# Optimization experiments

Hardware: AMD Instinct MI355X
Metric: run time of the kernel (lower is better)

## Reference

```python
import jax, jax.numpy as jnp
import numpy as np

D = 128
EPS = 1e-5

def group_norm1(x, gamma, beta):
    # GroupNorm with num_groups=1 over channel dim of [N, C]
    mu = jnp.mean(x, axis=-1, keepdims=True)
    var = jnp.mean(jnp.square(x - mu), axis=-1, keepdims=True)
    xhat = (x - mu) * jax.lax.rsqrt(var + EPS)
    return xhat * gamma + beta

def setup_inputs() -> dict:
    key = jax.random.key(0)
    ks = jax.random.split(key, 12)
    N_ctx, N_tgt, E = 40000, 40000, 640000
    s = 0.09  # ~1/sqrt(128) weight scale
    inp = {
        'context_feat': jax.random.normal(ks[0], (N_ctx, D), jnp.float32),
        'target_feat': jax.random.normal(ks[1], (N_tgt, D), jnp.float32),
        'context_pose': jax.random.normal(ks[2], (N_ctx, 4), jnp.float32),
        'target_pose': jax.random.normal(ks[3], (N_tgt, 4), jnp.float32),
        'W_input': s * jax.random.normal(ks[4], (D, D), jnp.float32),
        'W_rp': 0.5 * jax.random.normal(ks[5], (4, D), jnp.float32),
        'b_rp': jnp.zeros((D,), jnp.float32),
        'W_c1': s * jax.random.normal(ks[6], (2 * D, D), jnp.float32),
        'g_c1': jnp.ones((D,), jnp.float32),
        'b_c1': jnp.zeros((D,), jnp.float32),
        'W_c2': s * jax.random.normal(ks[7], (D, D), jnp.float32),
        'g_n': jnp.ones((D,), jnp.float32),
        'b_n': jnp.zeros((D,), jnp.float32),
        'W_m1': s * jax.random.normal(ks[8], (D, D), jnp.float32),
        'g_m1': jnp.ones((D,), jnp.float32),
        'bm1': jnp.zeros((D,), jnp.float32),
        'W_m2': s * jax.random.normal(ks[9], (D, D), jnp.float32),
        'g_m2': jnp.ones((D,), jnp.float32),
        'bm2': jnp.zeros((D,), jnp.float32),
        'hi': jax.random.randint(ks[10], (E,), 0, N_ctx, jnp.int32),
        'wi': jax.random.randint(ks[11], (E,), 0, N_tgt, jnp.int32),
    }
    return inp

def reference(context_feat, target_feat, context_pose, target_pose,
              W_input, W_rp, b_rp, W_c1, g_c1, b_c1, W_c2,
              g_n, b_n, W_m1, g_m1, bm1, W_m2, g_m2, bm2, hi, wi):
    # relpose: Linear(4,128) + ReLU on relative pose of each (context, target) edge
    dist_feat = context_pose[hi] - target_pose[wi]                 # [E, 4]
    dist_feat = jax.nn.relu(dist_feat @ W_rp + b_rp)               # [E, 128]
    # ctx: Linear(256,128,GN,ReLU) -> Linear(128,128, no bias)
    ctx = jnp.concatenate([context_feat[hi], dist_feat], axis=-1)  # [E, 256]
    ctx = jax.nn.relu(group_norm1(ctx @ W_c1, g_c1, b_c1))
    ctx = ctx @ W_c2                                               # [E, 128]
    # input linear + index_add scatter into targets
    tf = target_feat @ W_input                                     # [N_tgt, 128]
    tf = tf + jax.ops.segment_sum(ctx, wi, num_segments=target_feat.shape[0])
    tf = jax.nn.relu(group_norm1(tf, g_n, b_n))
    # mlp: Linear(GN,ReLU) -> Linear(GN, no act)
    tf = jax.nn.relu(group_norm1(tf @ W_m1, g_m1, bm1))
    tf = group_norm1(tf @ W_m2, g_m2, bm2)
    # residual + relu
    return jax.nn.relu(tf + target_feat)
```

## Files before the change

### kernel.cpp

```cpp
#include <hip/hip_runtime.h>

#define D 128
#define EPSV 1e-5f

typedef __attribute__((ext_vector_type(8))) __bf16 bf16x8;
typedef __attribute__((ext_vector_type(4))) float f32x4;

__device__ __forceinline__ ushort f2bf(float x) {
  unsigned u = __float_as_uint(x);
  u += 0x7fffu + ((u >> 16) & 1u);
  return (ushort)(u >> 16);
}
__device__ __forceinline__ unsigned cvtpk(float lo, float hi) {
  unsigned r;
  asm("v_cvt_pk_bf16_f32 %0, %1, %2" : "=v"(r) : "v"(lo), "v"(hi));
  return r;
}
__device__ __forceinline__ int yidx(int row, int col) {
  return row * 128 + (col ^ ((row & 7) << 3));
}

__global__ void k_cvt(const float* __restrict__ Wc1, const float* __restrict__ Wc2,
                      ushort* __restrict__ WF1, ushort* __restrict__ WF2) {
  int o = blockIdx.x * 256 + threadIdx.x;
  if (o < 32768) {
    int j = o & 7, col = (o >> 3) & 127, gg = (o >> 10) & 3, kc = o >> 12;
    WF1[o] = f2bf(Wc1[(kc * 32 + gg * 8 + j) * 128 + col]);
  } else {
    int o2 = o - 32768;
    if (o2 < 16384) {
      int j = o2 & 7, col = (o2 >> 3) & 127, gg = (o2 >> 10) & 3, kc = o2 >> 12;
      WF2[o2] = f2bf(Wc2[(kc * 32 + gg * 8 + j) * 128 + col]);
    }
  }
}

__global__ void k_cvtf(const float* __restrict__ cf, ushort* __restrict__ cb,
                       int n8) {
  int i = blockIdx.x * 256 + threadIdx.x;
  if (i < n8) {
    float4 f0 = *(const float4*)(cf + (size_t)i * 8);
    float4 f1 = *(const float4*)(cf + (size_t)i * 8 + 4);
    uint4 p;
    p.x = cvtpk(f0.x, f0.y); p.y = cvtpk(f0.z, f0.w);
    p.z = cvtpk(f1.x, f1.y); p.w = cvtpk(f1.z, f1.w);
    *(uint4*)(cb + (size_t)i * 8) = p;
  }
}

template <bool BF16CF>
__global__ __launch_bounds__(256, 4) void k_edge(
    const float* __restrict__ cfeat, const ushort* __restrict__ cfb,
    const float* __restrict__ cpose, const float* __restrict__ tpose,
    const float* __restrict__ Wrp, const float* __restrict__ brp,
    const float* __restrict__ gc1, const float* __restrict__ bc1,
    const ushort* __restrict__ WF1, const ushort* __restrict__ WF2,
    const int* __restrict__ hi, const int* __restrict__ wi,
    float* __restrict__ acc, int E) {
  __shared__ ushort Ybuf[128 * 128];
  __shared__ float gnbuf[2][128][2];
  __shared__ int wl[128];

  const int t = threadIdx.x;
  const int lane = t & 63;
  const int wv = t >> 6;
  const int wm = wv >> 1, wn = wv & 1;
  const int s = lane & 15, g = lane >> 4;
  const int e0 = blockIdx.x * 128;

  if (t < 128) wl[t] = wi[min(e0 + t, E - 1)];

  int hl[4];
#pragma unroll
  for (int m = 0; m < 4; ++m)
    hl[m] = hi[min(e0 + wm * 64 + m * 16 + s, E - 1)];

  {
    const int e = t >> 1;
    const int jh = (t & 1) * 64;
    const int ge = min(e0 + e, E - 1);
    const int h = hi[ge], w = wi[ge];
    float4 cp = *(const float4*)(cpose + (size_t)h * 4);
    float4 tp = *(const float4*)(tpose + (size_t)w * 4);
    const float d0 = cp.x - tp.x, d1 = cp.y - tp.y;
    const float d2 = cp.z - tp.z, d3 = cp.w - tp.w;
#pragma unroll
    for (int q = 0; q < 16; ++q) {
      const int j = jh + q * 4;
      float4 b  = *(const float4*)(brp + j);
      float4 w0 = *(const float4*)(Wrp + j);
      float4 w1 = *(const float4*)(Wrp + D + j);
      float4 w2 = *(const float4*)(Wrp + 2 * D + j);
      float4 w3 = *(const float4*)(Wrp + 3 * D + j);
      float r0 = fmaxf(b.x + d0 * w0.x + d1 * w1.x + d2 * w2.x + d3 * w3.x, 0.f);
      float r1 = fmaxf(b.y + d0 * w0.y + d1 * w1.y + d2 * w2.y + d3 * w3.y, 0.f);
      float r2 = fmaxf(b.z + d0 * w0.z + d1 * w1.z + d2 * w2.z + d3 * w3.z, 0.f);
      float r3 = fmaxf(b.w + d0 * w0.w + d1 * w1.w + d2 * w2.w + d3 * w3.w, 0.f);
      *(uint2*)&Ybuf[yidx(e, j)] = make_uint2(cvtpk(r0, r1), cvtpk(r2, r3));
    }
  }

  auto bfrag = [&](const ushort* WF, int kc, int n) {
    return *(const bf16x8*)&WF[(((kc * 4 + g) * 128) + wn * 64 + n * 16 + s) * 8];
  };

  f32x4 acc1[4][4];
#pragma unroll
  for (int m = 0; m < 4; ++m)
#pragma unroll
    for (int n = 0; n < 4; ++n) acc1[m][n] = (f32x4){0.f, 0.f, 0.f, 0.f};

  for (int kc = 0; kc < 4; ++kc) {
    bf16x8 a[4];
    if (BF16CF) {
#pragma unroll
      for (int m = 0; m < 4; ++m)
        a[m] = *(const bf16x8*)(cfb + (size_t)hl[m] * D + kc * 32 + g * 8);
    } else {
#pragma unroll
      for (int m = 0; m < 4; ++m) {
        const float* src = cfeat + (size_t)hl[m] * D + kc * 32 + g * 8;
        float4 f0 = *(const float4*)src;
        float4 f1 = *(const float4*)(src + 4);
        union { uint4 u; bf16x8 v; } cv;
        cv.u.x = cvtpk(f0.x, f0.y); cv.u.y = cvtpk(f0.z, f0.w);
        cv.u.z = cvtpk(f1.x, f1.y); cv.u.w = cvtpk(f1.z, f1.w);
        a[m] = cv.v;
      }
    }
#pragma unroll
    for (int n = 0; n < 4; ++n) {
      bf16x8 b = bfrag(WF1, kc, n);
#pragma unroll
      for (int m = 0; m < 4; ++m)
        acc1[m][n] =
            __builtin_amdgcn_mfma_f32_16x16x32_bf16(a[m], b, acc1[m][n], 0, 0, 0);
    }
  }

  __syncthreads();

  for (int kc = 4; kc < 8; ++kc) {
    bf16x8 a[4];
#pragma unroll
    for (int m = 0; m < 4; ++m)
      a[m] = *(const bf16x8*)
          &Ybuf[yidx(wm * 64 + m * 16 + s, (kc - 4) * 32 + g * 8)];
#pragma unroll
    for (int n = 0; n < 4; ++n) {
      bf16x8 b = bfrag(WF1, kc, n);
#pragma unroll
      for (int m = 0; m < 4; ++m)
        acc1[m][n] =
            __builtin_amdgcn_mfma_f32_16x16x32_bf16(a[m], b, acc1[m][n], 0, 0, 0);
    }
  }

#pragma unroll
  for (int m = 0; m < 4; ++m) {
#pragma unroll
    for (int reg = 0; reg < 4; ++reg) {
      float p1 = acc1[m][0][reg] + acc1[m][1][reg] + acc1[m][2][reg] +
                 acc1[m][3][reg];
      float p2 = acc1[m][0][reg] * acc1[m][0][reg] +
                 acc1[m][1][reg] * acc1[m][1][reg] +
                 acc1[m][2][reg] * acc1[m][2][reg] +
                 acc1[m][3][reg] * acc1[m][3][reg];
#pragma unroll
      for (int msk = 1; msk < 16; msk <<= 1) {
        p1 += __shfl_xor(p1, msk, 64);
        p2 += __shfl_xor(p2, msk, 64);
      }
      if (s == 0) {
        const int row = wm * 64 + m * 16 + g * 4 + reg;
        *(float2*)&gnbuf[wn][row][0] = make_float2(p1, p2);
      }
    }
  }
  __syncthreads();

  {
    float gcl[4], bcl[4];
#pragma unroll
    for (int n = 0; n < 4; ++n) {
      gcl[n] = gc1[wn * 64 + n * 16 + s];
      bcl[n] = bc1[wn * 64 + n * 16 + s];
    }
#pragma unroll
    for (int m = 0; m < 4; ++m) {
#pragma unroll
      for (int reg = 0; reg < 4; ++reg) {
        const int row = wm * 64 + m * 16 + g * 4 + reg;
        float2 q0 = *(const float2*)&gnbuf[0][row][0];
        float2 q1 = *(const float2*)&gnbuf[1][row][0];
        const float mean = (q0.x + q1.x) * (1.f / 128.f);
        const float var = (q0.y + q1.y) * (1.f / 128.f) - mean * mean;
        const float rstd = rsqrtf(var + EPSV);
#pragma unroll
        for (int n = 0; n < 4; ++n) {
          float y = fmaxf((acc1[m][n][reg] - mean) * rstd * gcl[n] + bcl[n], 0.f);
          Ybuf[yidx(row, wn * 64 + n * 16 + s)] = (ushort)cvtpk(y, y);
        }
      }
    }
  }
  __syncthreads();

  f32x4 acc2[4][4];
#pragma unroll
  for (int m = 0; m < 4; ++m)
#pragma unroll
    for (int n = 0; n < 4; ++n) acc2[m][n] = (f32x4){0.f, 0.f, 0.f, 0.f};

  for (int kc = 0; kc < 4; ++kc) {
    bf16x8 a[4];
#pragma unroll
    for (int m = 0; m < 4; ++m)
      a[m] = *(const bf16x8*)&Ybuf[yidx(wm * 64 + m * 16 + s, kc * 32 + g * 8)];
#pragma unroll
    for (int n = 0; n < 4; ++n) {
      bf16x8 b = bfrag(WF2, kc, n);
#pragma unroll
      for (int m = 0; m < 4; ++m)
        acc2[m][n] =
            __builtin_amdgcn_mfma_f32_16x16x32_bf16(a[m], b, acc2[m][n], 0, 0, 0);
    }
  }

#pragma unroll
  for (int m = 0; m < 4; ++m) {
#pragma unroll
    for (int reg = 0; reg < 4; ++reg) {
      const int rl = wm * 64 + m * 16 + g * 4 + reg;
      if (e0 + rl < E) {
        const int w = wl[rl];
        float* base = acc + (size_t)w * D + wn * 64 + s;
#pragma unroll
        for (int n = 0; n < 4; ++n)
          unsafeAtomicAdd(base + n * 16, acc2[m][n][reg]);
      }
    }
  }
}

__device__ __forceinline__ void reduce16(float& a, float& b) {
#pragma unroll
  for (int w = 1; w < 16; w <<= 1) {
    a += __shfl_xor(a, w, 64);
    b += __shfl_xor(b, w, 64);
  }
}

__global__ __launch_bounds__(256, 2) void k_input(
    const float* __restrict__ tfeat, const float* __restrict__ Wi,
    float* __restrict__ acc, int N) {
  __shared__ float Wbuf[64][132];
  __shared__ float xt[64][132];
  const int t = threadIdx.x;
  const int r = t >> 4, s = t & 15, j0 = s * 8;
  const int row0 = blockIdx.x * 64;

  for (int idx = t; idx < 64 * 32; idx += 256) {
    int rr = idx >> 5, c4 = idx & 31;
    int grow = row0 + rr;
    float4 v = make_float4(0.f, 0.f, 0.f, 0.f);
    if (grow < N) v = *(const float4*)(tfeat + (size_t)grow * D + c4 * 4);
    *(float4*)&xt[rr][c4 * 4] = v;
  }

  float a[4][8] = {};
  for (int kc = 0; kc < 2; ++kc) {
    __syncthreads();
    for (int idx = t; idx < 64 * 32; idx += 256) {
      int kk = idx >> 5, c4 = idx & 31;
      *(float4*)&Wbuf[kk][c4 * 4] =
          *(const float4*)(Wi + (size_t)(kc * 64 + kk) * D + c4 * 4);
    }
    __syncthreads();
#pragma unroll 4
    for (int kk = 0; kk < 64; ++kk) {
      float4 w0 = *(const float4*)&Wbuf[kk][j0];
      float4 w1 = *(const float4*)&Wbuf[kk][j0 + 4];
#pragma unroll
      for (int i = 0; i < 4; ++i) {
        float xv = xt[r + 16 * i][kc * 64 + kk];
        a[i][0] += xv * w0.x; a[i][1] += xv * w0.y;
        a[i][2] += xv * w0.z; a[i][3] += xv * w0.w;
        a[i][4] += xv * w1.x; a[i][5] += xv * w1.y;
        a[i][6] += xv * w1.z; a[i][7] += xv * w1.w;
      }
    }
  }
#pragma unroll
  for (int i = 0; i < 4; ++i) {
    int row = row0 + r + 16 * i;
    if (row < N) {
      *(float4*)(acc + (size_t)row * D + j0) =
          make_float4(a[i][0], a[i][1], a[i][2], a[i][3]);
      *(float4*)(acc + (size_t)row * D + j0 + 4) =
          make_float4(a[i][4], a[i][5], a[i][6], a[i][7]);
    }
  }
}

__global__ __launch_bounds__(256, 2) void k_node(
    const float* __restrict__ tfeat,
    const float* __restrict__ gn, const float* __restrict__ bn,
    const float* __restrict__ Wm1, const float* __restrict__ gm1,
    const float* __restrict__ bm1,
    const float* __restrict__ Wm2, const float* __restrict__ gm2,
    const float* __restrict__ bm2,
    float* __restrict__ acc, int N) {
  __shared__ float Wbuf[64][132];
  __shared__ float xt[64][132];
  const int t = threadIdx.x;
  const int r = t >> 4, s = t & 15, j0 = s * 8;
  const int row0 = blockIdx.x * 64;

  auto stageW = [&](const float* W, int kc) {
    for (int idx = t; idx < 64 * 32; idx += 256) {
      int kk = idx >> 5, c4 = idx & 31;
      *(float4*)&Wbuf[kk][c4 * 4] =
          *(const float4*)(W + (size_t)(kc * 64 + kk) * D + c4 * 4);
    }
  };
  auto gemm = [&](float (&a)[4][8], int kc) {
#pragma unroll 4
    for (int kk = 0; kk < 64; ++kk) {
      float4 w0 = *(const float4*)&Wbuf[kk][j0];
      float4 w1 = *(const float4*)&Wbuf[kk][j0 + 4];
#pragma unroll
      for (int i = 0; i < 4; ++i) {
        float xv = xt[r + 16 * i][kc * 64 + kk];
        a[i][0] += xv * w0.x; a[i][1] += xv * w0.y;
        a[i][2] += xv * w0.z; a[i][3] += xv * w0.w;
        a[i][4] += xv * w1.x; a[i][5] += xv * w1.y;
        a[i][6] += xv * w1.z; a[i][7] += xv * w1.w;
      }
    }
  };

  {
    float gv[8], bv[8];
#pragma unroll
    for (int m = 0; m < 8; ++m) { gv[m] = gn[j0 + m]; bv[m] = bn[j0 + m]; }
#pragma unroll
    for (int i = 0; i < 4; ++i) {
      int row = row0 + r + 16 * i;
      float v[8] = {};
      if (row < N) {
        float4 v0 = *(const float4*)(acc + (size_t)row * D + j0);
        float4 v1 = *(const float4*)(acc + (size_t)row * D + j0 + 4);
        v[0] = v0.x; v[1] = v0.y; v[2] = v0.z; v[3] = v0.w;
        v[4] = v1.x; v[5] = v1.y; v[6] = v1.z; v[7] = v1.w;
      }
      float s1 = 0.f, s2 = 0.f;
#pragma unroll
      for (int m = 0; m < 8; ++m) { s1 += v[m]; s2 += v[m] * v[m]; }
      reduce16(s1, s2);
      float mean = s1 * (1.f / 128.f);
      float var = s2 * (1.f / 128.f) - mean * mean;
      float rstd = rsqrtf(var + EPSV);
#pragma unroll
      for (int m = 0; m < 8; ++m)
        xt[r + 16 * i][j0 + m] = fmaxf((v[m] - mean) * rstd * gv[m] + bv[m], 0.f);
    }
  }

  float a[4][8] = {};
  for (int kc = 0; kc < 2; ++kc) {
    __syncthreads();
    stageW(Wm1, kc);
    __syncthreads();
    gemm(a, kc);
  }
  __syncthreads();
  {
    float gv[8], bv[8];
#pragma unroll
    for (int m = 0; m < 8; ++m) { gv[m] = gm1[j0 + m]; bv[m] = bm1[j0 + m]; }
#pragma unroll
    for (int i = 0; i < 4; ++i) {
      float s1 = 0.f, s2 = 0.f;
#pragma unroll
      for (int m = 0; m < 8; ++m) { s1 += a[i][m]; s2 += a[i][m] * a[i][m]; }
      reduce16(s1, s2);
      float mean = s1 * (1.f / 128.f);
      float var = s2 * (1.f / 128.f) - mean * mean;
      float rstd = rsqrtf(var + EPSV);
#pragma unroll
      for (int m = 0; m < 8; ++m)
        xt[r + 16 * i][j0 + m] =
            fmaxf((a[i][m] - mean) * rstd * gv[m] + bv[m], 0.f);
    }
  }

  float a2[4][8] = {};
  for (int kc = 0; kc < 2; ++kc) {
    __syncthreads();
    stageW(Wm2, kc);
    __syncthreads();
    gemm(a2, kc);
  }
  {
    float gv[8], bv[8];
#pragma unroll
    for (int m = 0; m < 8; ++m) { gv[m] = gm2[j0 + m]; bv[m] = bm2[j0 + m]; }
#pragma unroll
    for (int i = 0; i < 4; ++i) {
      int row = row0 + r + 16 * i;
      float s1 = 0.f, s2 = 0.f;
#pragma unroll
      for (int m = 0; m < 8; ++m) { s1 += a2[i][m]; s2 += a2[i][m] * a2[i][m]; }
      reduce16(s1, s2);
      float mean = s1 * (1.f / 128.f);
      float var = s2 * (1.f / 128.f) - mean * mean;
      float rstd = rsqrtf(var + EPSV);
      if (row < N) {
        float o[8];
#pragma unroll
        for (int m = 0; m < 8; ++m) {
          float x = (a2[i][m] - mean) * rstd * gv[m] + bv[m];
          o[m] = fmaxf(x + tfeat[(size_t)row * D + j0 + m], 0.f);
        }
        *(float4*)(acc + (size_t)row * D + j0) =
            make_float4(o[0], o[1], o[2], o[3]);
        *(float4*)(acc + (size_t)row * D + j0 + 4) =
            make_float4(o[4], o[5], o[6], o[7]);
      }
    }
  }
}

extern "C" void kernel_launch(void* const* d_in, const int* in_sizes, int n_in,
                              void* d_out, int out_size, void* d_ws,
                              size_t ws_size, hipStream_t stream) {
  const float* cfeat = (const float*)d_in[0];
  const float* tfeat = (const float*)d_in[1];
  const float* cpose = (const float*)d_in[2];
  const float* tpose = (const float*)d_in[3];
  const float* Wi    = (const float*)d_in[4];
  const float* Wrp   = (const float*)d_in[5];
  const float* brp   = (const float*)d_in[6];
  const float* Wc1   = (const float*)d_in[7];
  const float* gc1   = (const float*)d_in[8];
  const float* bc1   = (const float*)d_in[9];
  const float* Wc2   = (const float*)d_in[10];
  const float* gn    = (const float*)d_in[11];
  const float* bn    = (const float*)d_in[12];
  const float* Wm1   = (const float*)d_in[13];
  const float* gm1   = (const float*)d_in[14];
  const float* bm1   = (const float*)d_in[15];
  const float* Wm2   = (const float*)d_in[16];
  const float* gm2   = (const float*)d_in[17];
  const float* bm2   = (const float*)d_in[18];
  const int* hi      = (const int*)d_in[19];
  const int* wi      = (const int*)d_in[20];

  const int N = in_sizes[1] / D;
  const int E = in_sizes[19];
  const int CFE = in_sizes[0];
  float* out = (float*)d_out;

  uint8_t* ws = (uint8_t*)d_ws;
  ushort* WF1 = (ushort*)ws;
  ushort* WF2 = (ushort*)(ws + 65536);
  ushort* cfb = (ushort*)(ws + 98304);
  const bool bf16cf = ws_size >= 98304 + (size_t)CFE * 2;

  const int nbN = (N + 63) / 64;
  const int nbE = (E + 127) / 128;

  k_cvt<<<192, 256, 0, stream>>>(Wc1, Wc2, WF1, WF2);
  if (bf16cf) k_cvtf<<<(CFE / 8 + 255) / 256, 256, 0, stream>>>(cfeat, cfb, CFE / 8);
  k_input<<<nbN, 256, 0, stream>>>(tfeat, Wi, out, N);
  if (bf16cf)
    k_edge<true><<<nbE, 256, 0, stream>>>(cfeat, cfb, cpose, tpose, Wrp, brp,
                                          gc1, bc1, WF1, WF2, hi, wi, out, E);
  else
    k_edge<false><<<nbE, 256, 0, stream>>>(cfeat, cfb, cpose, tpose, Wrp, brp,
                                           gc1, bc1, WF1, WF2, hi, wi, out, E);
  k_node<<<nbN, 256, 0, stream>>>(tfeat, gn, bn, Wm1, gm1, bm1, Wm2, gm2, bm2,
                                  out, N);
}
```

Baseline: 476.3 us.

## Scatter pre-W_c2 activations in bf16 and apply W_c2 per node

Uses linearity of segment_sum: the edge kernel now scatters the post-GroupNorm ReLU activations with packed bf16 atomics into a zeroed node buffer S, instead of running the second 128x128 GEMM per edge and scattering fp32 atomics. The node kernel loads S, multiplies it by W_c2, and adds the input projection before the first GroupNorm. This removes one edge-level GEMM (E=640k rows versus N=40k) and halves the atomic traffic and count. The cost is bf16 accumulation precision in the atomics and an extra memset plus a node-level GEMM.

```diff
diff --git a/kernel.cpp b/kernel.cpp
--- a/kernel.cpp
+++ b/kernel.cpp
@@ -16,22 +16,18 @@
   asm("v_cvt_pk_bf16_f32 %0, %1, %2" : "=v"(r) : "v"(lo), "v"(hi));
   return r;
 }
+__device__ __forceinline__ float bf2f(ushort u) {
+  return __uint_as_float((unsigned)u << 16);
+}
 __device__ __forceinline__ int yidx(int row, int col) {
   return row * 128 + (col ^ ((row & 7) << 3));
 }
 
-__global__ void k_cvt(const float* __restrict__ Wc1, const float* __restrict__ Wc2,
-                      ushort* __restrict__ WF1, ushort* __restrict__ WF2) {
+__global__ void k_cvt(const float* __restrict__ Wc1, ushort* __restrict__ WF1) {
   int o = blockIdx.x * 256 + threadIdx.x;
   if (o < 32768) {
     int j = o & 7, col = (o >> 3) & 127, gg = (o >> 10) & 3, kc = o >> 12;
     WF1[o] = f2bf(Wc1[(kc * 32 + gg * 8 + j) * 128 + col]);
-  } else {
-    int o2 = o - 32768;
-    if (o2 < 16384) {
-      int j = o2 & 7, col = (o2 >> 3) & 127, gg = (o2 >> 10) & 3, kc = o2 >> 12;
-      WF2[o2] = f2bf(Wc2[(kc * 32 + gg * 8 + j) * 128 + col]);
-    }
   }
 }
 
@@ -54,9 +50,9 @@
     const float* __restrict__ cpose, const float* __restrict__ tpose,
     const float* __restrict__ Wrp, const float* __restrict__ brp,
     const float* __restrict__ gc1, const float* __restrict__ bc1,
-    const ushort* __restrict__ WF1, const ushort* __restrict__ WF2,
+    const ushort* __restrict__ WF1,
     const int* __restrict__ hi, const int* __restrict__ wi,
-    float* __restrict__ acc, int E) {
+    ushort* __restrict__ S, int E) {
   __shared__ ushort Ybuf[128 * 128];
   __shared__ float gnbuf[2][128][2];
   __shared__ int wl[128];
@@ -100,8 +96,8 @@
     }
   }
 
-  auto bfrag = [&](const ushort* WF, int kc, int n) {
-    return *(const bf16x8*)&WF[(((kc * 4 + g) * 128) + wn * 64 + n * 16 + s) * 8];
+  auto bfrag = [&](int kc, int n) {
+    return *(const bf16x8*)&WF1[(((kc * 4 + g) * 128) + wn * 64 + n * 16 + s) * 8];
   };
 
   f32x4 acc1[4][4];
@@ -130,7 +126,7 @@
     }
 #pragma unroll
     for (int n = 0; n < 4; ++n) {
-      bf16x8 b = bfrag(WF1, kc, n);
+      bf16x8 b = bfrag(kc, n);
 #pragma unroll
       for (int m = 0; m < 4; ++m)
         acc1[m][n] =
@@ -148,7 +144,7 @@
           &Ybuf[yidx(wm * 64 + m * 16 + s, (kc - 4) * 32 + g * 8)];
 #pragma unroll
     for (int n = 0; n < 4; ++n) {
-      bf16x8 b = bfrag(WF1, kc, n);
+      bf16x8 b = bfrag(kc, n);
 #pragma unroll
       for (int m = 0; m < 4; ++m)
         acc1[m][n] =
@@ -186,6 +182,7 @@
       gcl[n] = gc1[wn * 64 + n * 16 + s];
       bcl[n] = bc1[wn * 64 + n * 16 + s];
     }
+    const int odd = s & 1;
 #pragma unroll
     for (int m = 0; m < 4; ++m) {
 #pragma unroll
@@ -196,48 +193,27 @@
         const float mean = (q0.x + q1.x) * (1.f / 128.f);
         const float var = (q0.y + q1.y) * (1.f / 128.f) - mean * mean;
         const float rstd = rsqrtf(var + EPSV);
+        float yv[4], pv[4];
 #pragma unroll
         for (int n = 0; n < 4; ++n) {
-          float y = fmaxf((acc1[m][n][reg] - mean) * rstd * gcl[n] + bcl[n], 0.f);
-          Ybuf[yidx(row, wn * 64 + n * 16 + s)] = (ushort)cvtpk(y, y);
+          yv[n] = fmaxf((acc1[m][n][reg] - mean) * rstd * gcl[n] + bcl[n], 0.f);
+          pv[n] = __shfl_xor(yv[n], 1, 64);
         }
-      }
-    }
-  }
-  __syncthreads();
-
-  f32x4 acc2[4][4];
-#pragma unroll
-  for (int m = 0; m < 4; ++m)
-#pragma unroll
-    for (int n = 0; n < 4; ++n) acc2[m][n] = (f32x4){0.f, 0.f, 0.f, 0.f};
-
-  for (int kc = 0; kc < 4; ++kc) {
-    bf16x8 a[4];
-#pragma unroll
-    for (int m = 0; m < 4; ++m)
-      a[m] = *(const bf16x8*)&Ybuf[yidx(wm * 64 + m * 16 + s, kc * 32 + g * 8)];
-#pragma unroll
-    for (int n = 0; n < 4; ++n) {
-      bf16x8 b = bfrag(WF2, kc, n);
-#pragma unroll
-      for (int m = 0; m < 4; ++m)
-        acc2[m][n] =
-            __builtin_amdgcn_mfma_f32_16x16x32_bf16(a[m], b, acc2[m][n], 0, 0, 0);
-    }
-  }
-
-#pragma unroll
-  for (int m = 0; m < 4; ++m) {
-#pragma unroll
-    for (int reg = 0; reg < 4; ++reg) {
-      const int rl = wm * 64 + m * 16 + g * 4 + reg;
-      if (e0 + rl < E) {
-        const int w = wl[rl];
-        float* base = acc + (size_t)w * D + wn * 64 + s;
-#pragma unroll
-        for (int n = 0; n < 4; ++n)
-          unsafeAtomicAdd(base + n * 16, acc2[m][n][reg]);
+        if (e0 + row < E) {
+          const int w = wl[row];
+          float vA = odd ? yv[2] : yv[0], pA = odd ? pv[2] : pv[0];
+          float vB = odd ? yv[3] : yv[1], pB = odd ? pv[3] : pv[1];
+          unsigned dA = odd ? cvtpk(pA, vA) : cvtpk(vA, pA);
+          unsigned dB = odd ? cvtpk(pB, vB) : cvtpk(vB, pB);
+          const int colA = wn * 64 + (odd ? 32 : 0) + (s & ~1);
+          unsigned long long aA =
+              (unsigned long long)(S + (size_t)w * D + colA);
+          unsigned long long aB = aA + 32;
+          asm volatile("global_atomic_pk_add_bf16 %0, %1, off"
+                       :: "v"(aA), "v"(dA) : "memory");
+          asm volatile("global_atomic_pk_add_bf16 %0, %1, off"
+                       :: "v"(aB), "v"(dB) : "memory");
+        }
       }
     }
   }
@@ -304,7 +280,8 @@
 }
 
 __global__ __launch_bounds__(256, 2) void k_node(
-    const float* __restrict__ tfeat,
+    const float* __restrict__ tfeat, const ushort* __restrict__ S,
+    const float* __restrict__ Wc2,
     const float* __restrict__ gn, const float* __restrict__ bn,
     const float* __restrict__ Wm1, const float* __restrict__ gm1,
     const float* __restrict__ bm1,
@@ -339,46 +316,10 @@
       }
     }
   };
-
-  {
+  auto gnorm = [&](float (&a)[4][8], const float* gv_, const float* bv_) {
     float gv[8], bv[8];
 #pragma unroll
-    for (int m = 0; m < 8; ++m) { gv[m] = gn[j0 + m]; bv[m] = bn[j0 + m]; }
-#pragma unroll
-    for (int i = 0; i < 4; ++i) {
-      int row = row0 + r + 16 * i;
-      float v[8] = {};
-      if (row < N) {
-        float4 v0 = *(const float4*)(acc + (size_t)row * D + j0);
-        float4 v1 = *(const float4*)(acc + (size_t)row * D + j0 + 4);
-        v[0] = v0.x; v[1] = v0.y; v[2] = v0.z; v[3] = v0.w;
-        v[4] = v1.x; v[5] = v1.y; v[6] = v1.z; v[7] = v1.w;
-      }
-      float s1 = 0.f, s2 = 0.f;
-#pragma unroll
-      for (int m = 0; m < 8; ++m) { s1 += v[m]; s2 += v[m] * v[m]; }
-      reduce16(s1, s2);
-      float mean = s1 * (1.f / 128.f);
-      float var = s2 * (1.f / 128.f) - mean * mean;
-      float rstd = rsqrtf(var + EPSV);
-#pragma unroll
-      for (int m = 0; m < 8; ++m)
-        xt[r + 16 * i][j0 + m] = fmaxf((v[m] - mean) * rstd * gv[m] + bv[m], 0.f);
-    }
-  }
-
-  float a[4][8] = {};
-  for (int kc = 0; kc < 2; ++kc) {
-    __syncthreads();
-    stageW(Wm1, kc);
-    __syncthreads();
-    gemm(a, kc);
-  }
-  __syncthreads();
-  {
-    float gv[8], bv[8];
-#pragma unroll
-    for (int m = 0; m < 8; ++m) { gv[m] = gm1[j0 + m]; bv[m] = bm1[j0 + m]; }
+    for (int m = 0; m < 8; ++m) { gv[m] = gv_[j0 + m]; bv[m] = bv_[j0 + m]; }
 #pragma unroll
     for (int i = 0; i < 4; ++i) {
       float s1 = 0.f, s2 = 0.f;
@@ -393,7 +334,57 @@
         xt[r + 16 * i][j0 + m] =
             fmaxf((a[i][m] - mean) * rstd * gv[m] + bv[m], 0.f);
     }
-  }
+  };
+
+  for (int idx = t; idx < 64 * 16; idx += 256) {
+    int rr = idx >> 4, c8 = (idx & 15) * 8;
+    int grow = row0 + rr;
+    if (grow < N) {
+      uint4 p = *(const uint4*)(S + (size_t)grow * D + c8);
+      xt[rr][c8 + 0] = bf2f((ushort)(p.x & 0xffff));
+      xt[rr][c8 + 1] = bf2f((ushort)(p.x >> 16));
+      xt[rr][c8 + 2] = bf2f((ushort)(p.y & 0xffff));
+      xt[rr][c8 + 3] = bf2f((ushort)(p.y >> 16));
+      xt[rr][c8 + 4] = bf2f((ushort)(p.z & 0xffff));
+      xt[rr][c8 + 5] = bf2f((ushort)(p.z >> 16));
+      xt[rr][c8 + 6] = bf2f((ushort)(p.w & 0xffff));
+      xt[rr][c8 + 7] = bf2f((ushort)(p.w >> 16));
+    } else {
+#pragma unroll
+      for (int m = 0; m < 8; ++m) xt[rr][c8 + m] = 0.f;
+    }
+  }
+
+  float a0[4][8] = {};
+#pragma unroll
+  for (int i = 0; i < 4; ++i) {
+    int row = row0 + r + 16 * i;
+    if (row < N) {
+      float4 v0 = *(const float4*)(acc + (size_t)row * D + j0);
+      float4 v1 = *(const float4*)(acc + (size_t)row * D + j0 + 4);
+      a0[i][0] = v0.x; a0[i][1] = v0.y; a0[i][2] = v0.z; a0[i][3] = v0.w;
+      a0[i][4] = v1.x; a0[i][5] = v1.y; a0[i][6] = v1.z; a0[i][7] = v1.w;
+    }
+  }
+
+  for (int kc = 0; kc < 2; ++kc) {
+    __syncthreads();
+    stageW(Wc2, kc);
+    __syncthreads();
+    gemm(a0, kc);
+  }
+  __syncthreads();
+  gnorm(a0, gn, bn);
+
+  float a[4][8] = {};
+  for (int kc = 0; kc < 2; ++kc) {
+    __syncthreads();
+    stageW(Wm1, kc);
+    __syncthreads();
+    gemm(a, kc);
+  }
+  __syncthreads();
+  gnorm(a, gm1, bm1);
 
   float a2[4][8] = {};
   for (int kc = 0; kc < 2; ++kc) {
@@ -464,22 +455,25 @@
 
   uint8_t* ws = (uint8_t*)d_ws;
   ushort* WF1 = (ushort*)ws;
-  ushort* WF2 = (ushort*)(ws + 65536);
-  ushort* cfb = (ushort*)(ws + 98304);
-  const bool bf16cf = ws_size >= 98304 + (size_t)CFE * 2;
+  ushort* S   = (ushort*)(ws + 65536);
+  const size_t sBytes = (size_t)N * D * 2;
+  ushort* cfb = (ushort*)(ws + 65536 + sBytes);
+  const bool bf16cf = ws_size >= 65536 + sBytes + (size_t)CFE * 2;
 
   const int nbN = (N + 63) / 64;
   const int nbE = (E + 127) / 128;
 
-  k_cvt<<<192, 256, 0, stream>>>(Wc1, Wc2, WF1, WF2);
-  if (bf16cf) k_cvtf<<<(CFE / 8 + 255) / 256, 256, 0, stream>>>(cfeat, cfb, CFE / 8);
+  hipMemsetAsync(S, 0, sBytes, stream);
+  k_cvt<<<128, 256, 0, stream>>>(Wc1, WF1);
+  if (bf16cf)
+    k_cvtf<<<(CFE / 8 + 255) / 256, 256, 0, stream>>>(cfeat, cfb, CFE / 8);
   k_input<<<nbN, 256, 0, stream>>>(tfeat, Wi, out, N);
   if (bf16cf)
     k_edge<true><<<nbE, 256, 0, stream>>>(cfeat, cfb, cpose, tpose, Wrp, brp,
-                                          gc1, bc1, WF1, WF2, hi, wi, out, E);
+                                          gc1, bc1, WF1, hi, wi, S, E);
   else
     k_edge<false><<<nbE, 256, 0, stream>>>(cfeat, cfb, cpose, tpose, Wrp, brp,
-                                           gc1, bc1, WF1, WF2, hi, wi, out, E);
-  k_node<<<nbN, 256, 0, stream>>>(tfeat, gn, bn, Wm1, gm1, bm1, Wm2, gm2, bm2,
-                                  out, N);
-}
+                                           gc1, bc1, WF1, hi, wi, S, E);
+  k_node<<<nbN, 256, 0, stream>>>(tfeat, S, Wc2, gn, bn, Wm1, gm1, bm1,
+                                  Wm2, gm2, bm2, out, N);
+}
```

Result: slower. 503.9 us (+5.8%).

## Counting-sort edges by context index before the edge kernel

Applied to the files above, without the earlier changes.

Adds a histogram, three-pass prefix scan and scatter that reorder edges by source context index. The edge kernel then reads permuted hi/wi arrays, so gathers of context features and poses hit nearby rows and cache better. This costs six extra launches, a memset, atomics and extra workspace, and it moves the bf16 context copy to a later offset. The scatter order within a bucket is nondeterministic, so float accumulation order changes.

```diff
diff --git a/kernel.cpp b/kernel.cpp
--- a/kernel.cpp
+++ b/kernel.cpp
@@ -48,6 +48,66 @@
   }
 }
 
+__global__ void k_hist(const int* __restrict__ hi, int* __restrict__ hist, int E) {
+  int i = blockIdx.x * 256 + threadIdx.x;
+  if (i < E) atomicAdd(&hist[hi[i]], 1);
+}
+
+__global__ void k_scan1(const int* __restrict__ hist, int* __restrict__ bsum, int Nc) {
+  __shared__ int sd[256];
+  int t = threadIdx.x, i = blockIdx.x * 256 + t;
+  sd[t] = (i < Nc) ? hist[i] : 0;
+  __syncthreads();
+  for (int off = 128; off > 0; off >>= 1) {
+    if (t < off) sd[t] += sd[t + off];
+    __syncthreads();
+  }
+  if (t == 0) bsum[blockIdx.x] = sd[0];
+}
+
+__global__ void k_scan2(const int* __restrict__ bsum, int* __restrict__ bpre, int nc) {
+  __shared__ int sd[256];
+  int t = threadIdx.x;
+  int v = (t < nc) ? bsum[t] : 0;
+  sd[t] = v;
+  __syncthreads();
+  for (int off = 1; off < 256; off <<= 1) {
+    int x = (t >= off) ? sd[t - off] : 0;
+    __syncthreads();
+    sd[t] += x;
+    __syncthreads();
+  }
+  if (t < nc) bpre[t] = sd[t] - v;
+}
+
+__global__ void k_scan3(const int* __restrict__ hist, const int* __restrict__ bpre,
+                        int* __restrict__ cursor, int Nc) {
+  __shared__ int sd[256];
+  int t = threadIdx.x, i = blockIdx.x * 256 + t;
+  int v = (i < Nc) ? hist[i] : 0;
+  sd[t] = v;
+  __syncthreads();
+  for (int off = 1; off < 256; off <<= 1) {
+    int x = (t >= off) ? sd[t - off] : 0;
+    __syncthreads();
+    sd[t] += x;
+    __syncthreads();
+  }
+  if (i < Nc) cursor[i] = bpre[blockIdx.x] + sd[t] - v;
+}
+
+__global__ void k_order(const int* __restrict__ hi, const int* __restrict__ wi,
+                        int* __restrict__ cursor,
+                        int* __restrict__ hs, int* __restrict__ wt, int E) {
+  int i = blockIdx.x * 256 + threadIdx.x;
+  if (i < E) {
+    int h = hi[i];
+    int p = atomicAdd(&cursor[h], 1);
+    hs[p] = h;
+    wt[p] = wi[i];
+  }
+}
+
 template <bool BF16CF>
 __global__ __launch_bounds__(256, 4) void k_edge(
     const float* __restrict__ cfeat, const ushort* __restrict__ cfb,
@@ -55,7 +115,7 @@
     const float* __restrict__ Wrp, const float* __restrict__ brp,
     const float* __restrict__ gc1, const float* __restrict__ bc1,
     const ushort* __restrict__ WF1, const ushort* __restrict__ WF2,
-    const int* __restrict__ hi, const int* __restrict__ wi,
+    const int* __restrict__ he, const int* __restrict__ we,
     float* __restrict__ acc, int E) {
   __shared__ ushort Ybuf[128 * 128];
   __shared__ float gnbuf[2][128][2];
@@ -68,18 +128,18 @@
   const int s = lane & 15, g = lane >> 4;
   const int e0 = blockIdx.x * 128;
 
-  if (t < 128) wl[t] = wi[min(e0 + t, E - 1)];
+  if (t < 128) wl[t] = we[min(e0 + t, E - 1)];
 
   int hl[4];
 #pragma unroll
   for (int m = 0; m < 4; ++m)
-    hl[m] = hi[min(e0 + wm * 64 + m * 16 + s, E - 1)];
+    hl[m] = he[min(e0 + wm * 64 + m * 16 + s, E - 1)];
 
   {
     const int e = t >> 1;
     const int jh = (t & 1) * 64;
     const int ge = min(e0 + e, E - 1);
-    const int h = hi[ge], w = wi[ge];
+    const int h = he[ge], w = we[ge];
     float4 cp = *(const float4*)(cpose + (size_t)h * 4);
     float4 tp = *(const float4*)(tpose + (size_t)w * 4);
     const float d0 = cp.x - tp.x, d1 = cp.y - tp.y;
@@ -457,29 +517,56 @@
   const int* hi      = (const int*)d_in[19];
   const int* wi      = (const int*)d_in[20];
 
-  const int N = in_sizes[1] / D;
-  const int E = in_sizes[19];
+  const int N  = in_sizes[1] / D;
+  const int NC = in_sizes[0] / D;
+  const int E  = in_sizes[19];
   const int CFE = in_sizes[0];
   float* out = (float*)d_out;
 
   uint8_t* ws = (uint8_t*)d_ws;
   ushort* WF1 = (ushort*)ws;
   ushort* WF2 = (ushort*)(ws + 65536);
-  ushort* cfb = (ushort*)(ws + 98304);
-  const bool bf16cf = ws_size >= 98304 + (size_t)CFE * 2;
+  int* hist   = (int*)(ws + 98304);
+  int* cursor = hist + NC;
+  int* bsum   = cursor + NC;
+  int* bpre   = bsum + 256;
+  int* hs     = bpre + 256;
+  int* wt     = hs + E;
+  const size_t sort_end =
+      98304 + ((size_t)2 * NC + 512 + (size_t)2 * E) * 4;
+  ushort* cfb = (ushort*)(ws + ((sort_end + 255) & ~(size_t)255));
+  const size_t cfb_end = ((sort_end + 255) & ~(size_t)255) + (size_t)CFE * 2;
+
+  const int nchunksC = (NC + 255) / 256;
+  const bool sorted = (ws_size >= sort_end) && (nchunksC <= 256);
+  const bool bf16cf = ws_size >= cfb_end;
 
   const int nbN = (N + 63) / 64;
   const int nbE = (E + 127) / 128;
+  const int nbEthr = (E + 255) / 256;
+
+  if (sorted) {
+    hipMemsetAsync(hist, 0, (size_t)NC * 4, stream);
+    k_hist<<<nbEthr, 256, 0, stream>>>(hi, hist, E);
+    k_scan1<<<nchunksC, 256, 0, stream>>>(hist, bsum, NC);
+    k_scan2<<<1, 256, 0, stream>>>(bsum, bpre, nchunksC);
+    k_scan3<<<nchunksC, 256, 0, stream>>>(hist, bpre, cursor, NC);
+    k_order<<<nbEthr, 256, 0, stream>>>(hi, wi, cursor, hs, wt, E);
+  }
 
   k_cvt<<<192, 256, 0, stream>>>(Wc1, Wc2, WF1, WF2);
-  if (bf16cf) k_cvtf<<<(CFE / 8 + 255) / 256, 256, 0, stream>>>(cfeat, cfb, CFE / 8);
+  if (bf16cf)
+    k_cvtf<<<(CFE / 8 + 255) / 256, 256, 0, stream>>>(cfeat, cfb, CFE / 8);
   k_input<<<nbN, 256, 0, stream>>>(tfeat, Wi, out, N);
+
+  const int* he = sorted ? hs : hi;
+  const int* we = sorted ? wt : wi;
   if (bf16cf)
     k_edge<true><<<nbE, 256, 0, stream>>>(cfeat, cfb, cpose, tpose, Wrp, brp,
-                                          gc1, bc1, WF1, WF2, hi, wi, out, E);
+                                          gc1, bc1, WF1, WF2, he, we, out, E);
   else
     k_edge<false><<<nbE, 256, 0, stream>>>(cfeat, cfb, cpose, tpose, Wrp, brp,
-                                           gc1, bc1, WF1, WF2, hi, wi, out, E);
+                                           gc1, bc1, WF1, WF2, he, we, out, E);
   k_node<<<nbN, 256, 0, stream>>>(tfeat, gn, bn, Wm1, gm1, bm1, Wm2, gm2, bm2,
                                   out, N);
 }
```

Result: slower. 523.1 us (+9.8%).
